# Performance work log

Hardware: AMD Instinct MI355X
Metric: run time of the kernel (lower is better)

Reference implementation:

```python
import jax, jax.numpy as jnp
import numpy as np

D_EMB = 512
N_HEADS = 8
D_K = 64
D_V = 64
D_FF = 2048
N_LAYERS = 6
VOCAB = 32000
SRC_LEN = 512


def sin_enc_table(n_position, d):
    pos = jnp.arange(n_position, dtype=jnp.float32)[:, None]
    j = jnp.arange(d, dtype=jnp.float32)[None, :]
    angle = pos / jnp.power(10000.0, 2.0 * jnp.floor(j / 2.0) / d)
    return jnp.where((jnp.arange(d) % 2 == 0)[None, :], jnp.sin(angle), jnp.cos(angle))


def layer_norm(x, gamma, beta, eps=1e-5):
    mu = jnp.mean(x, axis=-1, keepdims=True)
    var = jnp.mean(jnp.square(x - mu), axis=-1, keepdims=True)
    return (x - mu) * jax.lax.rsqrt(var + eps) * gamma + beta


def setup_inputs() -> dict:
    key = jax.random.key(0)
    ks = jax.random.split(key, 20)
    s = 0.02
    L = N_LAYERS
    inp = {
        'enc_inputs': jax.random.randint(ks[0], (16, 512), 0, VOCAB),
        'emb': jax.random.normal(ks[1], (VOCAB, D_EMB), jnp.float32) * s,
        'Wq': jax.random.normal(ks[2], (L, N_HEADS * D_K, D_EMB), jnp.float32) * s,
        'bq': jnp.zeros((L, N_HEADS * D_K), jnp.float32),
        'Wk': jax.random.normal(ks[3], (L, N_HEADS * D_K, D_EMB), jnp.float32) * s,
        'bk': jnp.zeros((L, N_HEADS * D_K), jnp.float32),
        'Wv': jax.random.normal(ks[4], (L, N_HEADS * D_V, D_EMB), jnp.float32) * s,
        'bv': jnp.zeros((L, N_HEADS * D_V), jnp.float32),
        'Wo': jax.random.normal(ks[5], (L, D_EMB, N_HEADS * D_V), jnp.float32) * s,
        'bo': jnp.zeros((L, D_EMB), jnp.float32),
        'g1': jnp.ones((L, D_EMB), jnp.float32),
        'b1': jnp.zeros((L, D_EMB), jnp.float32),
        'Wc1': jax.random.normal(ks[6], (L, D_FF, D_EMB), jnp.float32) * s,
        'bc1': jnp.zeros((L, D_FF), jnp.float32),
        'Wc2': jax.random.normal(ks[7], (L, D_EMB, D_FF), jnp.float32) * s,
        'bc2': jnp.zeros((L, D_EMB), jnp.float32),
        'g2': jnp.ones((L, D_EMB), jnp.float32),
        'b2': jnp.zeros((L, D_EMB), jnp.float32),
    }
    return inp


def encoder_fwd(enc_inputs, emb, Wq, bq, Wk, bk, Wv, bv, Wo, bo, g1, b1, Wc1, bc1, Wc2, bc2, g2, b2):
    B, S = enc_inputs.shape
    pos_table = sin_enc_table(SRC_LEN + 1, D_EMB)  # frozen
    x = emb[enc_inputs] + pos_table[jnp.arange(1, S + 1)][None, :, :]
    # pad mask: True where key token == 0; broadcast over heads and queries
    pad = (enc_inputs == 0)[:, None, None, :]  # [B,1,1,S]
    scale = 1.0 / np.sqrt(D_K)
    attn_weights = []
    for l in range(N_LAYERS):
        residual = x
        q = (x @ Wq[l].T + bq[l]).reshape(B, S, N_HEADS, D_K).transpose(0, 2, 1, 3)
        k = (x @ Wk[l].T + bk[l]).reshape(B, S, N_HEADS, D_K).transpose(0, 2, 1, 3)
        v = (x @ Wv[l].T + bv[l]).reshape(B, S, N_HEADS, D_V).transpose(0, 2, 1, 3)
        scores = jnp.einsum('bhqd,bhkd->bhqk', q, k) * scale
        scores = jnp.where(pad, -1e9, scores)
        w = jax.nn.softmax(scores, axis=-1)
        ctx = jnp.einsum('bhqk,bhkd->bhqd', w, v)
        ctx = ctx.transpose(0, 2, 1, 3).reshape(B, S, N_HEADS * D_V)
        x = layer_norm(ctx @ Wo[l].T + bo[l] + residual, g1[l], b1[l])
        # position-wise FFN (conv1d k=1 == dense)
        h = jax.nn.relu(x @ Wc1[l].T + bc1[l])
        x = layer_norm(h @ Wc2[l].T + bc2[l] + x, g2[l], b2[l])
        attn_weights.append(w)
    return x, jnp.stack(attn_weights)


def reference(enc_inputs, emb, Wq, bq, Wk, bk, Wv, bv, Wo, bo, g1, b1, Wc1, bc1, Wc2, bc2, g2, b2):
    return encoder_fwd(enc_inputs, emb, Wq, bq, Wk, bk, Wv, bv, Wo, bo, g1, b1, Wc1, bc1, Wc2, bc2, g2, b2)
```

## Files before the change

### kernel.cpp

```cpp
#include <hip/hip_runtime.h>

typedef unsigned short u16;
typedef __attribute__((ext_vector_type(8))) short s16x8;
typedef __attribute__((ext_vector_type(4))) float f32x4;
typedef __attribute__((ext_vector_type(4))) unsigned short u16x4;

#define DEVI __device__ __forceinline__

DEVI float bf2f(u16 h) { union { unsigned u; float f; } v; v.u = ((unsigned)h) << 16; return v.f; }
DEVI u16 f2bf(float f) {
  union { unsigned u; float f; } v; v.f = f;
  unsigned u = v.u;
  unsigned r = (u + 0x7fffu + ((u >> 16) & 1u)) >> 16;
  return (u16)r;
}

DEVI f32x4 mfma16(s16x8 a, s16x8 b, f32x4 c) {
  return __builtin_amdgcn_mfma_f32_16x16x32_bf16(a, b, c, 0, 0, 0);
}

__global__ void cvt_kern(const float* __restrict__ in, u16* __restrict__ out, int n4) {
  for (int i = blockIdx.x * blockDim.x + threadIdx.x; i < n4; i += gridDim.x * blockDim.x) {
    f32x4 v = ((const f32x4*)in)[i];
    u16x4 o = { f2bf(v[0]), f2bf(v[1]), f2bf(v[2]), f2bf(v[3]) };
    ((u16x4*)out)[i] = o;
  }
}

__global__ void cvt_qkv_kern(const float* __restrict__ Wq, const float* __restrict__ Wk,
                             const float* __restrict__ Wv, u16* __restrict__ Wout) {
  int total = 6 * 1536 * 512 / 8;
  for (int idx = blockIdx.x * blockDim.x + threadIdx.x; idx < total; idx += gridDim.x * blockDim.x) {
    int c8 = idx & 63;
    int t = idx >> 6;
    int r = t % 1536, l = t / 1536;
    const float* src; int rr = r;
    if (r < 512) src = Wq;
    else if (r < 1024) { src = Wk; rr = r - 512; }
    else { src = Wv; rr = r - 1024; }
    const f32x4* p = (const f32x4*)(src + ((size_t)(l * 512 + rr) * 512) + c8 * 8);
    f32x4 a = p[0], b = p[1];
    u16x4 o0 = { f2bf(a[0]), f2bf(a[1]), f2bf(a[2]), f2bf(a[3]) };
    u16x4 o1 = { f2bf(b[0]), f2bf(b[1]), f2bf(b[2]), f2bf(b[3]) };
    u16x4* q = (u16x4*)(Wout + (size_t)idx * 8);
    q[0] = o0; q[1] = o1;
  }
}

__global__ void biasqkv_kern(const float* __restrict__ bq, const float* __restrict__ bk,
                             const float* __restrict__ bv, float* __restrict__ bout) {
  int i = blockIdx.x * 256 + threadIdx.x;
  if (i >= 6 * 1536) return;
  int l = i / 1536, r = i % 1536;
  float v = (r < 512) ? bq[l * 512 + r] : (r < 1024) ? bk[l * 512 + r - 512] : bv[l * 512 + r - 1024];
  bout[i] = v;
}

__global__ void embed_kern(const int* __restrict__ tok, const float* __restrict__ emb,
                           float* __restrict__ x, u16* __restrict__ xb) {
  int bs = blockIdx.x;
  int s = bs & 511;
  int t = threadIdx.x;
  int id = tok[bs];
  float pos = (float)(s + 1);
  int j0 = t * 4;
  f32x4 e = *(const f32x4*)(emb + (size_t)id * 512 + j0);
  f32x4 o; u16x4 ob;
  #pragma unroll
  for (int u = 0; u < 4; ++u) {
    int j = j0 + u;
    float expo = (float)(j & ~1) * (1.0f / 512.0f);
    float ang = pos / powf(10000.0f, expo);
    float pe = (j & 1) ? cosf(ang) : sinf(ang);
    float v = e[u] + pe;
    o[u] = v; ob[u] = f2bf(v);
  }
  *(f32x4*)(x + (size_t)bs * 512 + j0) = o;
  *(u16x4*)(xb + (size_t)bs * 512 + j0) = ob;
}

template <int WM, bool RELU, bool F32OUT>
__global__ __launch_bounds__(256, 2) void gemm_bs(const u16* __restrict__ A,
                                                  const u16* __restrict__ Bt,
                                                  const float* __restrict__ bias,
                                                  float* __restrict__ Pf, u16* __restrict__ Cb,
                                                  int N, int K, int nN) {
  constexpr int MF = WM / 16;
  constexpr int RPB = WM * 4;
  __shared__ __align__(16) u16 Bsw[128 * 256];

  const int chunkw = gridDim.x >> 3;
  const int wgid = (blockIdx.x & 7) * chunkw + (blockIdx.x >> 3);
  const int n = wgid % nN, m = wgid / nN;
  const int bn0 = n * 128, bm0 = m * RPB;

  const int tid = threadIdx.x, lane = tid & 63, wid = tid >> 6;
  const int l15 = lane & 15, lhi = lane >> 4;
  const int mrow0 = bm0 + wid * WM;

  f32x4 acc[MF][8];
  #pragma unroll
  for (int i = 0; i < MF; ++i)
    #pragma unroll
    for (int j = 0; j < 8; ++j)
      #pragma unroll
      for (int r = 0; r < 4; ++r) acc[i][j][r] = 0.0f;

  const u16* aB[MF];
  #pragma unroll
  for (int i = 0; i < MF; ++i)
    aB[i] = A + (size_t)(mrow0 + i * 16 + l15) * K + lhi * 8;

  const int rounds = K >> 8;
  for (int r = 0; r < rounds; ++r) {
    const int kb = r << 8;
    s16x8 tmp[16];
    #pragma unroll
    for (int c = 0; c < 16; ++c) {
      int cc = c * 256 + tid;
      int row = cc >> 5, col = cc & 31;
      tmp[c] = *(const s16x8*)(Bt + (size_t)(bn0 + row) * K + kb + col * 8);
    }
    __syncthreads();
    #pragma unroll
    for (int c = 0; c < 16; ++c) {
      int cc = c * 256 + tid;
      int row = cc >> 5, col = cc & 31;
      int byte = row * 512 + ((col * 16) ^ ((row & 7) << 4));
      *(s16x8*)((char*)Bsw + byte) = tmp[c];
    }
    __syncthreads();
    #pragma unroll
    for (int ks = 0; ks < 8; ++ks) {
      s16x8 af[MF], bf[8];
      #pragma unroll
      for (int i = 0; i < MF; ++i)
        af[i] = *(const s16x8*)(aB[i] + kb + ks * 32);
      #pragma unroll
      for (int j = 0; j < 8; ++j) {
        int row = j * 16 + l15;
        int byte = row * 512 + (((ks * 64) + lhi * 16) ^ ((row & 7) << 4));
        bf[j] = *(const s16x8*)((char*)Bsw + byte);
      }
      #pragma unroll
      for (int i = 0; i < MF; ++i)
        #pragma unroll
        for (int j = 0; j < 8; ++j)
          acc[i][j] = mfma16(af[i], bf[j], acc[i][j]);
    }
  }

  const int r0 = mrow0 + lhi * 4;
  const int c0 = bn0 + l15;
  #pragma unroll
  for (int i = 0; i < MF; ++i)
    #pragma unroll
    for (int j = 0; j < 8; ++j) {
      int col = c0 + j * 16;
      float bv = F32OUT ? 0.0f : bias[col];
      #pragma unroll
      for (int r = 0; r < 4; ++r) {
        int row = r0 + i * 16 + r;
        float v = acc[i][j][r] + bv;
        if (RELU) v = fmaxf(v, 0.0f);
        if (F32OUT) Pf[(size_t)row * N + col] = v;
        else Cb[(size_t)row * N + col] = f2bf(v);
      }
    }
}

__global__ void ln2_kern(const float* __restrict__ parts,
                         const float* __restrict__ bias, const float* __restrict__ resid,
                         const float* __restrict__ gam, const float* __restrict__ bet,
                         float* __restrict__ out, u16* __restrict__ outb) {
  int row = blockIdx.x * 4 + (threadIdx.x >> 6);
  int t = threadIdx.x & 63;
  size_t base = (size_t)row * 512;
  const f32x4* p0 = (const f32x4*)(parts + base);
  f32x4 v0 = p0[t], v1 = p0[t + 64];
  const f32x4* bp2 = (const f32x4*)bias;
  f32x4 bia = bp2[t], bib = bp2[t + 64];
  const f32x4* rp = (const f32x4*)(resid + base);
  f32x4 rr0 = rp[t], rr1 = rp[t + 64];
  #pragma unroll
  for (int u = 0; u < 4; ++u) { v0[u] += bia[u] + rr0[u]; v1[u] += bib[u] + rr1[u]; }

  float s = v0[0] + v0[1] + v0[2] + v0[3] + v1[0] + v1[1] + v1[2] + v1[3];
  float q = v0[0]*v0[0] + v0[1]*v0[1] + v0[2]*v0[2] + v0[3]*v0[3]
          + v1[0]*v1[0] + v1[1]*v1[1] + v1[2]*v1[2] + v1[3]*v1[3];
  #pragma unroll
  for (int d = 1; d < 64; d <<= 1) { s += __shfl_xor(s, d, 64); q += __shfl_xor(q, d, 64); }
  float mu = s * (1.0f / 512.0f);
  float var = q * (1.0f / 512.0f) - mu * mu;
  float rs = rsqrtf(var + 1e-5f);
  const f32x4* gp = (const f32x4*)gam;
  const f32x4* bp = (const f32x4*)bet;
  f32x4 ga = gp[t], gb = gp[t + 64], ba = bp[t], bb = bp[t + 64];
  f32x4 o0, o1; u16x4 ob0, ob1;
  #pragma unroll
  for (int u = 0; u < 4; ++u) {
    float a0 = (v0[u] - mu) * rs * ga[u] + ba[u];
    float a1 = (v1[u] - mu) * rs * gb[u] + bb[u];
    o0[u] = a0; o1[u] = a1; ob0[u] = f2bf(a0); ob1[u] = f2bf(a1);
  }
  f32x4* op = (f32x4*)(out + base);
  op[t] = o0; op[t + 64] = o1;
  u16x4* obp = (u16x4*)(outb + base);
  obp[t] = ob0; obp[t + 64] = ob1;
}

__global__ void vtrans_kern(const u16* __restrict__ QKV, u16* __restrict__ Vt) {
  int bx = blockIdx.x;
  int st = bx & 7, h = (bx >> 3) & 7, b = bx >> 6;
  int s0 = st * 64;
  __shared__ __align__(16) u16 tile[64][72];
  int t = threadIdx.x;
  for (int c = t; c < 512; c += 256) {
    int r = c >> 3, cc = (c & 7) << 3;
    *(s16x8*)&tile[r][cc] =
        *(const s16x8*)&QKV[(size_t)(b * 512 + s0 + r) * 1536 + 1024 + h * 64 + cc];
  }
  __syncthreads();
  for (int c = t; c < 512; c += 256) {
    int d = c >> 3, sc = (c & 7) << 3;
    s16x8 o;
    #pragma unroll
    for (int i2 = 0; i2 < 8; ++i2) o[i2] = (short)tile[sc + i2][d];
    *(s16x8*)&Vt[((size_t)(b * 8 + h) * 64 + d) * 512 + s0 + sc] = o;
  }
}

__global__ void attn_kern(const u16* __restrict__ QKV, const u16* __restrict__ Vt,
                          const int* __restrict__ tok,
                          float* __restrict__ wout, u16* __restrict__ ctxb) {
  int bx = blockIdx.x;
  int qt = bx & 15;
  int h = (bx >> 4) & 7;
  int b = bx >> 7;
  int tid = threadIdx.x;
  int lane = tid & 63, wid = tid >> 6;
  int l15 = lane & 15, lhi = lane >> 4;
  int m0 = qt * 32;

  __shared__ __align__(16) u16 Wl[32][520];
  __shared__ float pmask[512];
  __shared__ float redbuf[2][32][4];

  for (int c = tid; c < 512; c += 256)
    pmask[c] = (tok[b * 512 + c] == 0) ? 1.0f : 0.0f;

  s16x8 qf[2][2];
  const u16* qbase = QKV + (size_t)(b * 512 + m0) * 1536 + h * 64;
  #pragma unroll
  for (int i = 0; i < 2; ++i)
    #pragma unroll
    for (int kk = 0; kk < 2; ++kk)
      qf[i][kk] = *(const s16x8*)(qbase + (size_t)(i * 16 + l15) * 1536 + kk * 32 + lhi * 8);

  f32x4 sacc[2][8];
  #pragma unroll
  for (int i = 0; i < 2; ++i)
    #pragma unroll
    for (int j = 0; j < 8; ++j)
      #pragma unroll
      for (int r = 0; r < 4; ++r) sacc[i][j][r] = 0.0f;

  int c0 = wid * 128;
  const u16* kbase = QKV + (size_t)(b * 512 + c0) * 1536 + 512 + h * 64;
  #pragma unroll
  for (int j = 0; j < 8; ++j) {
    #pragma unroll
    for (int kk = 0; kk < 2; ++kk) {
      s16x8 kf = *(const s16x8*)(kbase + (size_t)(j * 16 + l15) * 1536 + kk * 32 + lhi * 8);
      sacc[0][j] = mfma16(qf[0][kk], kf, sacc[0][j]);
      sacc[1][j] = mfma16(qf[1][kk], kf, sacc[1][j]);
    }
  }
  __syncthreads();

  float rm[2][4], sm[2][4], gi[2][4];
  #pragma unroll
  for (int i = 0; i < 2; ++i)
    #pragma unroll
    for (int r = 0; r < 4; ++r) rm[i][r] = -3.0e38f;

  #pragma unroll
  for (int j = 0; j < 8; ++j) {
    float pm = pmask[c0 + j * 16 + l15];
    #pragma unroll
    for (int i = 0; i < 2; ++i)
      #pragma unroll
      for (int r = 0; r < 4; ++r) {
        float sv = sacc[i][j][r] * 0.125f;
        sv = (pm != 0.0f) ? -1.0e9f : sv;
        sacc[i][j][r] = sv;
        rm[i][r] = fmaxf(rm[i][r], sv);
      }
  }
  #pragma unroll
  for (int d = 1; d < 16; d <<= 1)
    #pragma unroll
    for (int i = 0; i < 2; ++i)
      #pragma unroll
      for (int r = 0; r < 4; ++r)
        rm[i][r] = fmaxf(rm[i][r], __shfl_xor(rm[i][r], d, 64));

  if (l15 == 0) {
    #pragma unroll
    for (int i = 0; i < 2; ++i)
      #pragma unroll
      for (int r = 0; r < 4; ++r)
        redbuf[0][i * 16 + lhi * 4 + r][wid] = rm[i][r];
  }
  __syncthreads();
  #pragma unroll
  for (int i = 0; i < 2; ++i)
    #pragma unroll
    for (int r = 0; r < 4; ++r) {
      int row = i * 16 + lhi * 4 + r;
      rm[i][r] = fmaxf(fmaxf(redbuf[0][row][0], redbuf[0][row][1]),
                       fmaxf(redbuf[0][row][2], redbuf[0][row][3]));
      sm[i][r] = 0.0f;
    }
  #pragma unroll
  for (int j = 0; j < 8; ++j)
    #pragma unroll
    for (int i = 0; i < 2; ++i)
      #pragma unroll
      for (int r = 0; r < 4; ++r) {
        float pv = __expf(sacc[i][j][r] - rm[i][r]);
        sacc[i][j][r] = pv;
        sm[i][r] += pv;
      }
  #pragma unroll
  for (int d = 1; d < 16; d <<= 1)
    #pragma unroll
    for (int i = 0; i < 2; ++i)
      #pragma unroll
      for (int r = 0; r < 4; ++r)
        sm[i][r] += __shfl_xor(sm[i][r], d, 64);
  if (l15 == 0) {
    #pragma unroll
    for (int i = 0; i < 2; ++i)
      #pragma unroll
      for (int r = 0; r < 4; ++r)
        redbuf[1][i * 16 + lhi * 4 + r][wid] = sm[i][r];
  }
  __syncthreads();
  #pragma unroll
  for (int i = 0; i < 2; ++i)
    #pragma unroll
    for (int r = 0; r < 4; ++r) {
      int row = i * 16 + lhi * 4 + r;
      float tot = redbuf[1][row][0] + redbuf[1][row][1] + redbuf[1][row][2] + redbuf[1][row][3];
      gi[i][r] = 1.0f / tot;
    }

  #pragma unroll
  for (int j = 0; j < 8; ++j)
    #pragma unroll
    for (int i = 0; i < 2; ++i)
      #pragma unroll
      for (int r = 0; r < 4; ++r)
        Wl[i * 16 + lhi * 4 + r][c0 + j * 16 + l15] = f2bf(sacc[i][j][r] * gi[i][r]);
  __syncthreads();

  float* wrow = wout + ((size_t)((b * 8 + h) * 512 + m0)) * 512;
  for (int c = tid; c < 2048; c += 256) {
    int rr = c >> 6;
    int cc = (c & 63) << 3;
    s16x8 wv = *(const s16x8*)&Wl[rr][cc];
    f32x4 f0 = { bf2f((u16)wv[0]), bf2f((u16)wv[1]), bf2f((u16)wv[2]), bf2f((u16)wv[3]) };
    f32x4 f1 = { bf2f((u16)wv[4]), bf2f((u16)wv[5]), bf2f((u16)wv[6]), bf2f((u16)wv[7]) };
    *(f32x4*)(wrow + (size_t)rr * 512 + cc) = f0;
    *(f32x4*)(wrow + (size_t)rr * 512 + cc + 4) = f1;
  }

  f32x4 cacc[2];
  #pragma unroll
  for (int i = 0; i < 2; ++i)
    #pragma unroll
    for (int r = 0; r < 4; ++r) cacc[i][r] = 0.0f;
  const u16* vbase = Vt + ((size_t)((b * 8 + h) * 64 + wid * 16 + l15)) * 512;
  #pragma unroll
  for (int kk = 0; kk < 16; ++kk) {
    s16x8 vf = *(const s16x8*)(vbase + kk * 32 + lhi * 8);
    #pragma unroll
    for (int i = 0; i < 2; ++i) {
      s16x8 wf = *(const s16x8*)&Wl[i * 16 + l15][kk * 32 + lhi * 8];
      cacc[i] = mfma16(wf, vf, cacc[i]);
    }
  }
  #pragma unroll
  for (int i = 0; i < 2; ++i)
    #pragma unroll
    for (int r = 0; r < 4; ++r)
      ctxb[(size_t)(b * 512 + m0 + i * 16 + lhi * 4 + r) * 512 + h * 64 + wid * 16 + l15] =
          f2bf(cacc[i][r]);
}

extern "C" void kernel_launch(void* const* d_in, const int* in_sizes, int n_in,
                              void* d_out, int out_size, void* d_ws, size_t ws_size,
                              hipStream_t stream) {
  const int*   tok = (const int*)d_in[0];
  const float* emb = (const float*)d_in[1];
  const float* Wq  = (const float*)d_in[2];
  const float* bq  = (const float*)d_in[3];
  const float* Wk  = (const float*)d_in[4];
  const float* bk  = (const float*)d_in[5];
  const float* Wv  = (const float*)d_in[6];
  const float* bv  = (const float*)d_in[7];
  const float* Wo  = (const float*)d_in[8];
  const float* bo  = (const float*)d_in[9];
  const float* g1  = (const float*)d_in[10];
  const float* b1  = (const float*)d_in[11];
  const float* Wc1 = (const float*)d_in[12];
  const float* bc1 = (const float*)d_in[13];
  const float* Wc2 = (const float*)d_in[14];
  const float* bc2 = (const float*)d_in[15];
  const float* g2  = (const float*)d_in[16];
  const float* b2  = (const float*)d_in[17];
  (void)in_sizes; (void)n_in; (void)out_size; (void)ws_size;

  float* out_x = (float*)d_out;
  float* out_w = out_x + (size_t)16 * 512 * 512;

  char* p = (char*)d_ws;
  size_t off = 0;
  auto alloc = [&](size_t bytes) { char* r = p + off; off += (bytes + 255) & ~(size_t)255; return r; };
  u16*   xb  = (u16*)alloc((size_t)8192 * 512 * 2);
  float* xf  = (float*)alloc((size_t)8192 * 512 * 4);
  float* parts = (float*)alloc((size_t)8192 * 512 * 4);
  char*  regA = alloc((size_t)8192 * 1536 * 2 + (size_t)8192 * 512 * 2);
  u16* QKVb = (u16*)regA;
  u16* Vtb  = QKVb + (size_t)8192 * 1536;
  u16* hb   = (u16*)regA;
  u16* ctxb = (u16*)alloc((size_t)8192 * 512 * 2);
  u16* Wqkvb = (u16*)alloc((size_t)6 * 1536 * 512 * 2);
  u16* Wob   = (u16*)alloc((size_t)6 * 512 * 512 * 2);
  u16* Wc1b  = (u16*)alloc((size_t)6 * 2048 * 512 * 2);
  u16* Wc2b  = (u16*)alloc((size_t)6 * 2048 * 512 * 2);
  float* bqkvb = (float*)alloc((size_t)6 * 1536 * 4);

  cvt_qkv_kern<<<1024, 256, 0, stream>>>(Wq, Wk, Wv, Wqkvb);
  biasqkv_kern<<<36, 256, 0, stream>>>(bq, bk, bv, bqkvb);
  cvt_kern<<<1024, 256, 0, stream>>>(Wo,  Wob,  6 * 512 * 512 / 4);
  cvt_kern<<<1024, 256, 0, stream>>>(Wc1, Wc1b, 6 * 2048 * 512 / 4);
  cvt_kern<<<1024, 256, 0, stream>>>(Wc2, Wc2b, 6 * 2048 * 512 / 4);

  embed_kern<<<8192, 128, 0, stream>>>(tok, emb, xf, xb);

  for (int l = 0; l < 6; ++l) {
    const u16* wqkv_l = Wqkvb + (size_t)l * 1536 * 512;
    const u16* wo_l = Wob + (size_t)l * 512 * 512;
    const u16* w1_l = Wc1b + (size_t)l * 2048 * 512;
    const u16* w2_l = Wc2b + (size_t)l * 2048 * 512;

    gemm_bs<32, false, false><<<768, 256, 0, stream>>>(xb, wqkv_l, bqkvb + l * 1536,
                                                       nullptr, QKVb, 1536, 512, 12);
    vtrans_kern<<<1024, 256, 0, stream>>>(QKVb, Vtb);
    attn_kern<<<2048, 256, 0, stream>>>(QKVb, Vtb, tok,
                                        out_w + (size_t)l * 8 * 16 * 512 * 512, ctxb);
    gemm_bs<16, false, true><<<512, 256, 0, stream>>>(ctxb, wo_l, nullptr,
                                                      parts, nullptr, 512, 512, 4);
    ln2_kern<<<2048, 256, 0, stream>>>(parts, bo + l * 512, xf,
                                       g1 + l * 512, b1 + l * 512, xf, xb);
    gemm_bs<32, true, false><<<1024, 256, 0, stream>>>(xb, w1_l, bc1 + l * 2048,
                                                       nullptr, hb, 2048, 512, 16);
    gemm_bs<16, false, true><<<512, 256, 0, stream>>>(hb, w2_l, nullptr,
                                                      parts, nullptr, 512, 2048, 4);
    ln2_kern<<<2048, 256, 0, stream>>>(parts, bc2 + l * 512, xf,
                                       g2 + l * 512, b2 + l * 512, (l == 5 ? out_x : xf), xb);
  }
}
```

Baseline: 1.178 ms.

## Store projection outputs in bf16, write attention weights directly, swizzle attention grid

The Wo and FFN2 GEMMs now fold in their bias and write bf16 instead of fp32 partials, and the layernorm kernel reads those bf16 values, which halves that intermediate traffic. The attention kernel writes fp32 softmax weights straight from registers instead of staging them through LDS and a second copy loop. Attention block indices are remapped so neighbouring blocks go to different XCDs. The trade-offs are extra rounding of pre-LayerNorm values to bf16 and scattered, uncoalesced 4-byte stores of the attention weights.

```diff
diff --git a/kernel.cpp b/kernel.cpp
--- a/kernel.cpp
+++ b/kernel.cpp
@@ -79,11 +79,11 @@
   *(u16x4*)(xb + (size_t)bs * 512 + j0) = ob;
 }
 
-template <int WM, bool RELU, bool F32OUT>
+template <int WM, bool RELU>
 __global__ __launch_bounds__(256, 2) void gemm_bs(const u16* __restrict__ A,
                                                   const u16* __restrict__ Bt,
                                                   const float* __restrict__ bias,
-                                                  float* __restrict__ Pf, u16* __restrict__ Cb,
+                                                  u16* __restrict__ Cb,
                                                   int N, int K, int nN) {
   constexpr int MF = WM / 16;
   constexpr int RPB = WM * 4;
@@ -157,33 +157,34 @@
     #pragma unroll
     for (int j = 0; j < 8; ++j) {
       int col = c0 + j * 16;
-      float bv = F32OUT ? 0.0f : bias[col];
+      float bv = bias[col];
       #pragma unroll
       for (int r = 0; r < 4; ++r) {
         int row = r0 + i * 16 + r;
         float v = acc[i][j][r] + bv;
         if (RELU) v = fmaxf(v, 0.0f);
-        if (F32OUT) Pf[(size_t)row * N + col] = v;
-        else Cb[(size_t)row * N + col] = f2bf(v);
+        Cb[(size_t)row * N + col] = f2bf(v);
       }
     }
 }
 
-__global__ void ln2_kern(const float* __restrict__ parts,
-                         const float* __restrict__ bias, const float* __restrict__ resid,
+__global__ void ln2_kern(const u16* __restrict__ parts,
+                         const float* __restrict__ resid,
                          const float* __restrict__ gam, const float* __restrict__ bet,
                          float* __restrict__ out, u16* __restrict__ outb) {
   int row = blockIdx.x * 4 + (threadIdx.x >> 6);
   int t = threadIdx.x & 63;
   size_t base = (size_t)row * 512;
-  const f32x4* p0 = (const f32x4*)(parts + base);
-  f32x4 v0 = p0[t], v1 = p0[t + 64];
-  const f32x4* bp2 = (const f32x4*)bias;
-  f32x4 bia = bp2[t], bib = bp2[t + 64];
+  const u16x4* pp = (const u16x4*)(parts + base);
+  u16x4 pa = pp[t], pb4 = pp[t + 64];
   const f32x4* rp = (const f32x4*)(resid + base);
   f32x4 rr0 = rp[t], rr1 = rp[t + 64];
-  #pragma unroll
-  for (int u = 0; u < 4; ++u) { v0[u] += bia[u] + rr0[u]; v1[u] += bib[u] + rr1[u]; }
+  f32x4 v0, v1;
+  #pragma unroll
+  for (int u = 0; u < 4; ++u) {
+    v0[u] = bf2f(pa[u]) + rr0[u];
+    v1[u] = bf2f(pb4[u]) + rr1[u];
+  }
 
   float s = v0[0] + v0[1] + v0[2] + v0[3] + v1[0] + v1[1] + v1[2] + v1[3];
   float q = v0[0]*v0[0] + v0[1]*v0[1] + v0[2]*v0[2] + v0[3]*v0[3]
@@ -233,10 +234,10 @@
 __global__ void attn_kern(const u16* __restrict__ QKV, const u16* __restrict__ Vt,
                           const int* __restrict__ tok,
                           float* __restrict__ wout, u16* __restrict__ ctxb) {
-  int bx = blockIdx.x;
-  int qt = bx & 15;
-  int h = (bx >> 4) & 7;
-  int b = bx >> 7;
+  int wg = (blockIdx.x & 7) * 256 + (blockIdx.x >> 3);
+  int qt = wg & 15;
+  int h = (wg >> 4) & 7;
+  int b = wg >> 7;
   int tid = threadIdx.x;
   int lane = tid & 63, wid = tid >> 6;
   int l15 = lane & 15, lhi = lane >> 4;
@@ -356,25 +357,20 @@
       gi[i][r] = 1.0f / tot;
     }
 
+  float* wrow = wout + ((size_t)((b * 8 + h) * 512 + m0)) * 512;
   #pragma unroll
   for (int j = 0; j < 8; ++j)
     #pragma unroll
     for (int i = 0; i < 2; ++i)
       #pragma unroll
-      for (int r = 0; r < 4; ++r)
-        Wl[i * 16 + lhi * 4 + r][c0 + j * 16 + l15] = f2bf(sacc[i][j][r] * gi[i][r]);
+      for (int r = 0; r < 4; ++r) {
+        float wv = sacc[i][j][r] * gi[i][r];
+        int row = i * 16 + lhi * 4 + r;
+        int col = c0 + j * 16 + l15;
+        Wl[row][col] = f2bf(wv);
+        wrow[(size_t)row * 512 + col] = wv;
+      }
   __syncthreads();
-
-  float* wrow = wout + ((size_t)((b * 8 + h) * 512 + m0)) * 512;
-  for (int c = tid; c < 2048; c += 256) {
-    int rr = c >> 6;
-    int cc = (c & 63) << 3;
-    s16x8 wv = *(const s16x8*)&Wl[rr][cc];
-    f32x4 f0 = { bf2f((u16)wv[0]), bf2f((u16)wv[1]), bf2f((u16)wv[2]), bf2f((u16)wv[3]) };
-    f32x4 f1 = { bf2f((u16)wv[4]), bf2f((u16)wv[5]), bf2f((u16)wv[6]), bf2f((u16)wv[7]) };
-    *(f32x4*)(wrow + (size_t)rr * 512 + cc) = f0;
-    *(f32x4*)(wrow + (size_t)rr * 512 + cc + 4) = f1;
-  }
 
   f32x4 cacc[2];
   #pragma unroll
@@ -430,7 +426,7 @@
   auto alloc = [&](size_t bytes) { char* r = p + off; off += (bytes + 255) & ~(size_t)255; return r; };
   u16*   xb  = (u16*)alloc((size_t)8192 * 512 * 2);
   float* xf  = (float*)alloc((size_t)8192 * 512 * 4);
-  float* parts = (float*)alloc((size_t)8192 * 512 * 4);
+  u16*   pwo = (u16*)alloc((size_t)8192 * 512 * 2);
   char*  regA = alloc((size_t)8192 * 1536 * 2 + (size_t)8192 * 512 * 2);
   u16* QKVb = (u16*)regA;
   u16* Vtb  = QKVb + (size_t)8192 * 1536;
@@ -441,12 +437,16 @@
   u16* Wc1b  = (u16*)alloc((size_t)6 * 2048 * 512 * 2);
   u16* Wc2b  = (u16*)alloc((size_t)6 * 2048 * 512 * 2);
   float* bqkvb = (float*)alloc((size_t)6 * 1536 * 4);
+  float* bwo   = (float*)alloc((size_t)6 * 512 * 4);
+  float* bw2   = (float*)alloc((size_t)6 * 512 * 4);
 
   cvt_qkv_kern<<<1024, 256, 0, stream>>>(Wq, Wk, Wv, Wqkvb);
   biasqkv_kern<<<36, 256, 0, stream>>>(bq, bk, bv, bqkvb);
   cvt_kern<<<1024, 256, 0, stream>>>(Wo,  Wob,  6 * 512 * 512 / 4);
   cvt_kern<<<1024, 256, 0, stream>>>(Wc1, Wc1b, 6 * 2048 * 512 / 4);
   cvt_kern<<<1024, 256, 0, stream>>>(Wc2, Wc2b, 6 * 2048 * 512 / 4);
+  hipMemcpyAsync(bwo, bo, 6 * 512 * 4, hipMemcpyDeviceToDevice, stream);
+  hipMemcpyAsync(bw2, bc2, 6 * 512 * 4, hipMemcpyDeviceToDevice, stream);
 
   embed_kern<<<8192, 128, 0, stream>>>(tok, emb, xf, xb);
 
@@ -456,20 +456,19 @@
     const u16* w1_l = Wc1b + (size_t)l * 2048 * 512;
     const u16* w2_l = Wc2b + (size_t)l * 2048 * 512;
 
-    gemm_bs<32, false, false><<<768, 256, 0, stream>>>(xb, wqkv_l, bqkvb + l * 1536,
-                                                       nullptr, QKVb, 1536, 512, 12);
+    gemm_bs<32, false><<<768, 256, 0, stream>>>(xb, wqkv_l, bqkvb + l * 1536,
+                                                QKVb, 1536, 512, 12);
     vtrans_kern<<<1024, 256, 0, stream>>>(QKVb, Vtb);
     attn_kern<<<2048, 256, 0, stream>>>(QKVb, Vtb, tok,
                                         out_w + (size_t)l * 8 * 16 * 512 * 512, ctxb);
-    gemm_bs<16, false, true><<<512, 256, 0, stream>>>(ctxb, wo_l, nullptr,
-                                                      parts, nullptr, 512, 512, 4);
-    ln2_kern<<<2048, 256, 0, stream>>>(parts, bo + l * 512, xf,
-                                       g1 + l * 512, b1 + l * 512, xf, xb);
-    gemm_bs<32, true, false><<<1024, 256, 0, stream>>>(xb, w1_l, bc1 + l * 2048,
-                                                       nullptr, hb, 2048, 512, 16);
-    gemm_bs<16, false, true><<<512, 256, 0, stream>>>(hb, w2_l, nullptr,
-                                                      parts, nullptr, 512, 2048, 4);
-    ln2_kern<<<2048, 256, 0, stream>>>(parts, bc2 + l * 512, xf,
-                                       g2 + l * 512, b2 + l * 512, (l == 5 ? out_x : xf), xb);
-  }
-}
+    gemm_bs<16, false><<<512, 256, 0, stream>>>(ctxb, wo_l, bwo + l * 512,
+                                                pwo, 512, 512, 4);
+    ln2_kern<<<2048, 256, 0, stream>>>(pwo, xf, g1 + l * 512, b1 + l * 512, xf, xb);
+    gemm_bs<32, true><<<1024, 256, 0, stream>>>(xb, w1_l, bc1 + l * 2048,
+                                                hb, 2048, 512, 16);
+    gemm_bs<16, false><<<512, 256, 0, stream>>>(hb, w2_l, bw2 + l * 512,
+                                                pwo, 512, 2048, 4);
+    ln2_kern<<<2048, 256, 0, stream>>>(pwo, xf, g2 + l * 512, b2 + l * 512,
+                                       (l == 5 ? out_x : xf), xb);
+  }
+}
```

New measurement: 1.090 ms. 1.08x faster.
